# Kernel optimization log

Measured on AMD Instinct MI355X. Metric: run time of the kernel, lower is better.

## Reference

```python
import jax, jax.numpy as jnp
import numpy as np

HEADS = 8
DIM_HEAD = 64
EPS = 1e-05


def _layernorm(t, scale):
    # flax LayerNorm with use_bias=False: (t - mean) / sqrt(var + eps) * scale
    mu = jnp.mean(t, axis=-1, keepdims=True)
    var = jnp.var(t, axis=-1, keepdims=True)
    return (t - mu) * jax.lax.rsqrt(var + EPS) * scale


def setup_inputs() -> dict:
    key = jax.random.key(0)
    ks = jax.random.split(key, 5)
    B, H, W, C = 32, 32, 32, 512
    dim = HEADS * DIM_HEAD  # 512
    x = jax.random.normal(ks[0], (B, H, W, C), dtype=jnp.float32)
    ln1_scale = jnp.ones((C,), dtype=jnp.float32)
    # 1x1 convs == channel matmuls; kernels stored as [in, out]
    w_qkv = jax.random.normal(ks[1], (C, dim * 3), dtype=jnp.float32) * 0.02
    w_out = jax.random.normal(ks[2], (dim, C), dtype=jnp.float32) * 0.02
    b_out = jnp.zeros((C,), dtype=jnp.float32)
    ln2_scale = jnp.ones((C,), dtype=jnp.float32)
    return {"x": x, "ln1_scale": ln1_scale, "w_qkv": w_qkv,
            "w_out": w_out, "b_out": b_out, "ln2_scale": ln2_scale}


def reference(x, ln1_scale, w_qkv, w_out, b_out, ln2_scale):
    B, H, W, C = x.shape
    N = H * W
    dim = HEADS * DIM_HEAD

    normed = _layernorm(x, ln1_scale)                       # [B,H,W,C]
    qkv = jnp.einsum('bxyc,cf->bxyf', normed, w_qkv)        # 1x1 conv, no bias
    q, k, v = jnp.split(qkv, 3, axis=-1)
    q = q.reshape(B, N, HEADS, DIM_HEAD)
    k = k.reshape(B, N, HEADS, DIM_HEAD)
    v = v.reshape(B, N, HEADS, DIM_HEAD)

    q = jax.nn.softmax(q, axis=-1) / jnp.sqrt(jnp.asarray(DIM_HEAD, x.dtype))
    k = jax.nn.softmax(k, axis=1)   # softmax over the token axis (axis=-3)
    v = v / N

    # linear attention: context = k^T v, then out = q . context
    context = jnp.einsum('bnhd,bnhe->bhde', k, v)           # [B,h,d,e]
    out = jnp.einsum('bhde,bnhd->bnhe', context, q)         # == 'b h e n' transposed
    out = out.reshape(B, H, W, dim)

    out = jnp.einsum('bxyf,fc->bxyc', out, w_out) + b_out   # 1x1 conv with bias
    out = _layernorm(out, ln2_scale)                        # to_out.norm_0
    return out + x
```

## Files before the change

kernel.cpp:

```cpp
#include <hip/hip_runtime.h>
#include <stdint.h>

typedef _Float16 h8 __attribute__((ext_vector_type(8)));
typedef _Float16 h4v __attribute__((ext_vector_type(4)));
typedef float f32x4 __attribute__((ext_vector_type(4)));

__device__ __forceinline__ float clampf(float x, float lo, float hi) {
    return fminf(fmaxf(x, lo), hi);
}
__device__ __forceinline__ void gload16(const _Float16* g, _Float16* l) {
    __builtin_amdgcn_global_load_lds(
        (const __attribute__((address_space(1))) unsigned int*)g,
        (__attribute__((address_space(3))) unsigned int*)l, 16, 0, 0);
}

__global__ __launch_bounds__(256) void transpose_f2h(const float* __restrict__ in,
                                                     _Float16* __restrict__ out,
                                                     int rows, int cols) {
    __shared__ _Float16 tile[32][33];
    int bx = blockIdx.x * 32, by = blockIdx.y * 32;
    int tx = threadIdx.x & 31, ty = threadIdx.x >> 5;
    for (int i = ty; i < 32; i += 8)
        tile[i][tx] = (_Float16)in[(size_t)(by + i) * cols + bx + tx];
    __syncthreads();
    for (int i = ty; i < 32; i += 8)
        out[(size_t)(bx + i) * rows + by + tx] = tile[tx][i];
}

__global__ __launch_bounds__(256) void ln1_kernel(const float* __restrict__ x,
                                                  const float* __restrict__ scale,
                                                  _Float16* __restrict__ out) {
    int row = blockIdx.x * 4 + (threadIdx.x >> 6);
    int lane = threadIdx.x & 63;
    const float4* xp = (const float4*)(x + (size_t)row * 512 + lane * 8);
    float4 a = xp[0], b = xp[1];
    const float4* sp = (const float4*)(scale + lane * 8);
    float4 s0v = sp[0], s1v = sp[1];
    float f[8] = {a.x, a.y, a.z, a.w, b.x, b.y, b.z, b.w};
    float sc[8] = {s0v.x, s0v.y, s0v.z, s0v.w, s1v.x, s1v.y, s1v.z, s1v.w};
    float s = 0.f, ss = 0.f;
#pragma unroll
    for (int j = 0; j < 8; j++) { s += f[j]; ss += f[j] * f[j]; }
#pragma unroll
    for (int off = 1; off < 64; off <<= 1) { s += __shfl_xor(s, off); ss += __shfl_xor(ss, off); }
    float mean = s * (1.f / 512.f);
    float var  = ss * (1.f / 512.f) - mean * mean;
    float rs   = rsqrtf(fmaxf(var, 0.f) + 1e-5f);
    union { uint4 u; _Float16 h[8]; } ov;
#pragma unroll
    for (int j = 0; j < 8; j++) ov.h[j] = (_Float16)((f[j] - mean) * rs * sc[j]);
    *(uint4*)(out + (size_t)row * 512 + lane * 8) = ov.u;
}

__global__ __launch_bounds__(512) void gemm_kvexp(const _Float16* __restrict__ A,
                                                  const _Float16* __restrict__ BT,
                                                  _Float16* __restrict__ ekT,
                                                  _Float16* __restrict__ vT,
                                                  float* __restrict__ Sbuf) {
    __shared__ __attribute__((aligned(16))) _Float16 Ws[128 * 32];
    __shared__ __attribute__((aligned(16))) _Float16 Ns[512 * 32];
    int t = threadIdx.x, w = t >> 6, lane = t & 63;
    int lm = lane & 15, q4 = lane >> 4;
    int n0 = blockIdx.x * 512, c0 = blockIdx.y * 128;
    int wc = (w & 1) * 64, wn = (w >> 1) * 128;
    f32x4 acc[4][8];
#pragma unroll
    for (int i = 0; i < 4; i++)
#pragma unroll
        for (int j = 0; j < 8; j++) acc[i][j] = (f32x4){0.f, 0.f, 0.f, 0.f};

    int sr = t >> 2, sc = (t & 3) * 8;
    const _Float16* Wg = BT + (size_t)(c0 + sr) * 512 + sc;
    const _Float16* Ng = A + (size_t)(n0 + sr) * 512 + sc;
    _Float16* WsW = Ws + w * 512;

    for (int k0 = 0; k0 < 512; k0 += 32) {
        gload16(Wg + k0, WsW);
#pragma unroll
        for (int j = 0; j < 4; j++)
            gload16(Ng + (size_t)j * 128 * 512 + k0, Ns + j * 4096 + w * 512);
        __syncthreads();
        h8 wf[4], nf[8];
#pragma unroll
        for (int i = 0; i < 4; i++) wf[i] = *(const h8*)(Ws + (wc + i * 16 + lm) * 32 + q4 * 8);
#pragma unroll
        for (int i = 0; i < 8; i++) nf[i] = *(const h8*)(Ns + (wn + i * 16 + lm) * 32 + q4 * 8);
#pragma unroll
        for (int ci = 0; ci < 4; ci++)
#pragma unroll
            for (int nj = 0; nj < 8; nj++)
                acc[ci][nj] = __builtin_amdgcn_mfma_f32_16x16x32_f16(nf[nj], wf[ci], acc[ci][nj], 0, 0, 0);
        __syncthreads();
    }
    bool isK = (c0 < 512);
    int bl = n0 >> 10;
    int nl0 = (n0 & 1023) + wn;
    _Float16* obase = isK ? ekT : vT;
#pragma unroll
    for (int ci = 0; ci < 4; ci++) {
        int c_abs = c0 + wc + ci * 16 + lm;
        int h = (c_abs >> 6) & 7, de = c_abs & 63;
        _Float16* rowp = obase + ((size_t)(bl * 8 + h) * 64 + de) * 1024 + nl0;
        float ssum = 0.f;
#pragma unroll
        for (int nj = 0; nj < 8; nj++) {
            f32x4 v = acc[ci][nj];
            h4v o;
#pragma unroll
            for (int r = 0; r < 4; r++) {
                float f = v[r];
                if (isK) f = __expf(clampf(f, -30.f, 30.f));
                _Float16 e = (_Float16)f;
                o[r] = e;
                ssum += (float)e;
            }
            *(h4v*)(rowp + nj * 16 + q4 * 4) = o;
        }
        if (isK) {
            ssum += __shfl_xor(ssum, 16);
            ssum += __shfl_xor(ssum, 32);
            if (q4 == 0) atomicAdd(&Sbuf[(bl * 8 + h) * 64 + de], ssum);
        }
    }
}

__global__ __launch_bounds__(512) void ctx_gemm(const _Float16* __restrict__ ekT,
                                                const _Float16* __restrict__ vT,
                                                float* __restrict__ part) {
    __shared__ __attribute__((aligned(16))) _Float16 As[64 * 32];
    __shared__ __attribute__((aligned(16))) _Float16 Bs[64 * 32];
    int t = threadIdx.x, w = t >> 6, lane = t & 63;
    int lm = lane & 15, q4 = lane >> 4;
    int bhl = blockIdx.x;
    int wd = (w & 3) * 16, we = (w >> 2) * 32;
    int tl = t & 255;
    int sr = tl >> 2, sc = (tl & 3) * 8;
    const _Float16* G = (t >= 256 ? vT : ekT) + (size_t)bhl * 65536 + (size_t)sr * 1024 + sc;
    _Float16* LW = (t >= 256 ? Bs : As) + (w & 3) * 512;
    f32x4 acc[2];
    acc[0] = (f32x4){0.f, 0.f, 0.f, 0.f};
    acc[1] = (f32x4){0.f, 0.f, 0.f, 0.f};

    for (int k0 = 0; k0 < 1024; k0 += 32) {
        gload16(G + k0, LW);
        __syncthreads();
        h8 af = *(const h8*)(As + (wd + lm) * 32 + q4 * 8);
#pragma unroll
        for (int nt = 0; nt < 2; nt++) {
            h8 bf = *(const h8*)(Bs + (we + nt * 16 + lm) * 32 + q4 * 8);
            acc[nt] = __builtin_amdgcn_mfma_f32_16x16x32_f16(bf, af, acc[nt], 0, 0, 0);
        }
        __syncthreads();
    }
    float* dst = part + (size_t)bhl * 4096 + (wd + lm) * 64 + we;
#pragma unroll
    for (int nt = 0; nt < 2; nt++)
        *(f32x4*)(dst + nt * 16 + q4 * 4) = acc[nt];
}

__global__ __launch_bounds__(256) void gemm_qattn(const _Float16* __restrict__ A,
                                                  const _Float16* __restrict__ BT,
                                                  const float* __restrict__ part,
                                                  const float* __restrict__ Sbuf,
                                                  _Float16* __restrict__ attn) {
    __shared__ __attribute__((aligned(16))) char smem[33792 + 17408];
    _Float16* As  = (_Float16*)smem;
    _Float16* Bs  = (_Float16*)(smem + 8192);
    _Float16* qn  = (_Float16*)smem;
    _Float16* csT = (_Float16*)(smem + 33792);
    int t = threadIdx.x, w = t >> 6, lane = t & 63;
    int lm = lane & 15, q4 = lane >> 4;
    int m0 = blockIdx.y * 128, n0 = blockIdx.x * 128;
    int wm = (w & 1) * 64, wn = (w >> 1) * 64;
    f32x4 acc[4][4];
#pragma unroll
    for (int i = 0; i < 4; i++)
#pragma unroll
        for (int j = 0; j < 4; j++) acc[i][j] = (f32x4){0.f, 0.f, 0.f, 0.f};

    int sr = t >> 2, sc = (t & 3) * 8;
    const _Float16* Ag = A + (size_t)(m0 + sr) * 512 + sc;
    const _Float16* Bg = BT + (size_t)(n0 + sr) * 512 + sc;
    _Float16* AsW = As + w * 512;
    _Float16* BsW = Bs + w * 512;

    for (int k0 = 0; k0 < 512; k0 += 32) {
        gload16(Ag + k0, AsW);
        gload16(Ag + (size_t)64 * 512 + k0, AsW + 64 * 32);
        gload16(Bg + k0, BsW);
        gload16(Bg + (size_t)64 * 512 + k0, BsW + 64 * 32);
        __syncthreads();
        h8 af[4], bf[4];
#pragma unroll
        for (int i = 0; i < 4; i++) af[i] = *(const h8*)(As + (wm + i * 16 + lm) * 32 + q4 * 8);
#pragma unroll
        for (int i = 0; i < 4; i++) bf[i] = *(const h8*)(Bs + (wn + i * 16 + lm) * 32 + q4 * 8);
#pragma unroll
        for (int mi = 0; mi < 4; mi++)
#pragma unroll
            for (int ni = 0; ni < 4; ni++)
                acc[mi][ni] = __builtin_amdgcn_mfma_f32_16x16x32_f16(bf[ni], af[mi], acc[mi][ni], 0, 0, 0);
        __syncthreads();
    }
    float rws[4];
#pragma unroll
    for (int mi = 0; mi < 4; mi++) {
        float s = 0.f;
#pragma unroll
        for (int ni = 0; ni < 4; ni++) {
            f32x4 e;
#pragma unroll
            for (int r = 0; r < 4; r++) {
                e[r] = __expf(clampf(acc[mi][ni][r], -30.f, 30.f));
                s += e[r];
            }
            acc[mi][ni] = e;
        }
        s += __shfl_xor(s, 16);
        s += __shfl_xor(s, 32);
        rws[mi] = 1.f / (s * 8.f);
    }
#pragma unroll
    for (int mi = 0; mi < 4; mi++) {
        int row = wm + mi * 16 + lm;
        float r = rws[mi];
#pragma unroll
        for (int ni = 0; ni < 4; ni++) {
            int col0 = wn + ni * 16 + q4 * 4;
            h4v o;
#pragma unroll
            for (int j = 0; j < 4; j++) o[j] = (_Float16)(acc[mi][ni][j] * r);
            *(h4v*)(qn + row * 132 + col0) = o;
        }
    }
    int bl = m0 >> 10;
    int head0 = n0 >> 6;
#pragma unroll
    for (int hh2 = 0; hh2 < 2; hh2++) {
        int bh = bl * 8 + head0 + hh2;
        const f32x4* p0 = (const f32x4*)(part + (size_t)bh * 4096);
        for (int i = t; i < 1024; i += 256) {
            f32x4 v = p0[i];
            int d = i >> 4, e0 = (i & 15) * 4;
            float is = 1.f / Sbuf[bh * 64 + d];
#pragma unroll
            for (int j = 0; j < 4; j++)
                csT[hh2 * 64 * 68 + (e0 + j) * 68 + d] = (_Float16)(v[j] * is);
        }
    }
    __syncthreads();
    int hh = w >> 1;
    f32x4 acc2[4][4];
#pragma unroll
    for (int i = 0; i < 4; i++)
#pragma unroll
        for (int j = 0; j < 4; j++) acc2[i][j] = (f32x4){0.f, 0.f, 0.f, 0.f};
#pragma unroll
    for (int kc = 0; kc < 2; kc++) {
        h8 af[4], bf[4];
#pragma unroll
        for (int mi = 0; mi < 4; mi++) {
            const _Float16* p = qn + (wm + mi * 16 + lm) * 132 + hh * 64 + kc * 32 + q4 * 8;
            h4v lo = *(const h4v*)p;
            h4v hi = *(const h4v*)(p + 4);
            h8 a;
#pragma unroll
            for (int j = 0; j < 4; j++) { a[j] = lo[j]; a[4 + j] = hi[j]; }
            af[mi] = a;
        }
#pragma unroll
        for (int ni = 0; ni < 4; ni++) {
            const _Float16* p = csT + hh * 64 * 68 + (ni * 16 + lm) * 68 + kc * 32 + q4 * 8;
            h4v lo = *(const h4v*)p;
            h4v hi = *(const h4v*)(p + 4);
            h8 b;
#pragma unroll
            for (int j = 0; j < 4; j++) { b[j] = lo[j]; b[4 + j] = hi[j]; }
            bf[ni] = b;
        }
#pragma unroll
        for (int mi = 0; mi < 4; mi++)
#pragma unroll
            for (int ni = 0; ni < 4; ni++)
                acc2[mi][ni] = __builtin_amdgcn_mfma_f32_16x16x32_f16(bf[ni], af[mi], acc2[mi][ni], 0, 0, 0);
    }
#pragma unroll
    for (int mi = 0; mi < 4; mi++) {
        int row = m0 + wm + mi * 16 + lm;
#pragma unroll
        for (int ni = 0; ni < 4; ni++) {
            int col0 = n0 + wn + ni * 16 + q4 * 4;
            h4v o;
#pragma unroll
            for (int r = 0; r < 4; r++) o[r] = (_Float16)acc2[mi][ni][r];
            *(h4v*)(attn + (size_t)row * 512 + col0) = o;
        }
    }
}

__global__ __launch_bounds__(512) void gemm_projln2(const _Float16* __restrict__ A,
                                                    const _Float16* __restrict__ BT,
                                                    const float* __restrict__ bias,
                                                    const float* __restrict__ x,
                                                    const float* __restrict__ scale,
                                                    float* __restrict__ out) {
    __shared__ __attribute__((aligned(16))) _Float16 As[128 * 32];
    __shared__ __attribute__((aligned(16))) _Float16 Bs[512 * 32];
    __shared__ float rs_sum[2][64][4];
    __shared__ float rs_ssq[2][64][4];
    int t = threadIdx.x, w = t >> 6, lane = t & 63;
    int lm = lane & 15, q4 = lane >> 4;
    int m0 = blockIdx.x * 128;
    int wm = (w & 1) * 64, wn = (w >> 1) * 128;
    f32x4 acc[4][8];
#pragma unroll
    for (int i = 0; i < 4; i++)
#pragma unroll
        for (int j = 0; j < 8; j++) acc[i][j] = (f32x4){0.f, 0.f, 0.f, 0.f};

    int sr = t >> 2, sc = (t & 3) * 8;
    const _Float16* Ag = A + (size_t)(m0 + sr) * 512 + sc;
    const _Float16* Bg = BT + (size_t)sr * 512 + sc;
    _Float16* AsW = As + w * 512;

    for (int k0 = 0; k0 < 512; k0 += 32) {
        gload16(Ag + k0, AsW);
#pragma unroll
        for (int j = 0; j < 4; j++)
            gload16(Bg + (size_t)j * 128 * 512 + k0, Bs + j * 4096 + w * 512);
        __syncthreads();
        h8 af[4], bf[8];
#pragma unroll
        for (int i = 0; i < 4; i++) af[i] = *(const h8*)(As + (wm + i * 16 + lm) * 32 + q4 * 8);
#pragma unroll
        for (int i = 0; i < 8; i++) bf[i] = *(const h8*)(Bs + (wn + i * 16 + lm) * 32 + q4 * 8);
#pragma unroll
        for (int mi = 0; mi < 4; mi++)
#pragma unroll
            for (int ni = 0; ni < 8; ni++)
                acc[mi][ni] = __builtin_amdgcn_mfma_f32_16x16x32_f16(bf[ni], af[mi], acc[mi][ni], 0, 0, 0);
        __syncthreads();
    }
    const float os = 1.f / 1024.f;
    int mwi = w & 1, nwi = w >> 1;
#pragma unroll
    for (int mi = 0; mi < 4; mi++) {
        float s = 0.f, ss = 0.f;
#pragma unroll
        for (int ni = 0; ni < 8; ni++) {
            float4 b4 = *(const float4*)(bias + wn + ni * 16 + q4 * 4);
            const float* bp = &b4.x;
#pragma unroll
            for (int r = 0; r < 4; r++) {
                float v = acc[mi][ni][r] * os + bp[r];
                acc[mi][ni][r] = v;
                s += v; ss += v * v;
            }
        }
        s  += __shfl_xor(s, 16);  s  += __shfl_xor(s, 32);
        ss += __shfl_xor(ss, 16); ss += __shfl_xor(ss, 32);
        if (q4 == 0) {
            rs_sum[mwi][mi * 16 + lm][nwi] = s;
            rs_ssq[mwi][mi * 16 + lm][nwi] = ss;
        }
    }
    __syncthreads();
#pragma unroll
    for (int mi = 0; mi < 4; mi++) {
        int r64 = mi * 16 + lm;
        float s  = rs_sum[mwi][r64][0] + rs_sum[mwi][r64][1] + rs_sum[mwi][r64][2] + rs_sum[mwi][r64][3];
        float ss = rs_ssq[mwi][r64][0] + rs_ssq[mwi][r64][1] + rs_ssq[mwi][r64][2] + rs_ssq[mwi][r64][3];
        float mean = s * (1.f / 512.f);
        float var  = ss * (1.f / 512.f) - mean * mean;
        float rstd = rsqrtf(fmaxf(var, 0.f) + 1e-5f);
        int row = m0 + wm + r64;
#pragma unroll
        for (int ni = 0; ni < 8; ni++) {
            int col0 = wn + ni * 16 + q4 * 4;
            float4 sc4 = *(const float4*)(scale + col0);
            float4 x4  = *(const float4*)(x + (size_t)row * 512 + col0);
            const float* scp = &sc4.x; const float* xp = &x4.x;
            float4 o;
            float* op = &o.x;
#pragma unroll
            for (int r = 0; r < 4; r++)
                op[r] = (acc[mi][ni][r] - mean) * rstd * scp[r] + xp[r];
            *(float4*)(out + (size_t)row * 512 + col0) = o;
        }
    }
}

extern "C" void kernel_launch(void* const* d_in, const int* in_sizes, int n_in,
                              void* d_out, int out_size, void* d_ws, size_t ws_size,
                              hipStream_t stream) {
    const float* x    = (const float*)d_in[0];
    const float* ln1s = (const float*)d_in[1];
    const float* wqkv = (const float*)d_in[2];
    const float* wout = (const float*)d_in[3];
    const float* bout = (const float*)d_in[4];
    const float* ln2s = (const float*)d_in[5];
    float* out = (float*)d_out;

    char* ws = (char*)d_ws;
    _Float16* wqkvT  = (_Float16*)(ws);
    _Float16* woutT  = (_Float16*)(ws + 1572864);
    float*    part   = (float*)(ws + 2097152);
    float*    Sbuf   = (float*)(ws + 6291456);
    _Float16* normed = (_Float16*)(ws + 6356992);
    _Float16* attnF  = (_Float16*)(ws + 39911424);
    _Float16* ekT = (_Float16*)d_out;
    _Float16* vT  = (_Float16*)((char*)d_out + 33554432);

    transpose_f2h<<<dim3(48, 16), 256, 0, stream>>>(wqkv, wqkvT, 512, 1536);
    transpose_f2h<<<dim3(16, 16), 256, 0, stream>>>(wout, woutT, 512, 512);
    ln1_kernel<<<8192, 256, 0, stream>>>(x, ln1s, normed);
    hipMemsetAsync(Sbuf, 0, 65536, stream);

    gemm_kvexp<<<dim3(64, 8), 512, 0, stream>>>(normed, wqkvT + 512 * 512, ekT, vT, Sbuf);
    ctx_gemm<<<256, 512, 0, stream>>>(ekT, vT, part);
    gemm_qattn<<<dim3(4, 256), 256, 0, stream>>>(normed, wqkvT, part, Sbuf, attnF);
    gemm_projln2<<<256, 512, 0, stream>>>(attnF, woutT, bout, x, ln2s, out);
}
```

Before: 290.7 us.

## Fuse K/V projection with context GemM and shrink projection-LN2 tiles

The K/V projection GEMM now computes exp(k) and v for one batch-head over a 512-token chunk. It writes them as fp16 into shared memory and immediately accumulates the k^T v context with MFMA, so the separate ctx_gemm kernel and the 64 MB fp16 ekT/vT round trip through global memory go away. Each of the two token chunks writes its own context partial, and gemm_qattn sums the two. The output projection + LayerNorm kernel now uses 64-row tiles across 512 blocks instead of 128-row tiles, trading more redundant weight loads for better occupancy and a smaller accumulator footprint. The fused kernel also adds extra barriers and a serialized 4-chunk staging loop in shared memory.

```diff
diff --git a/kernel.cpp b/kernel.cpp
--- a/kernel.cpp
+++ b/kernel.cpp
@@ -52,16 +52,19 @@
     *(uint4*)(out + (size_t)row * 512 + lane * 8) = ov.u;
 }
 
-__global__ __launch_bounds__(512) void gemm_kvexp(const _Float16* __restrict__ A,
+__global__ __launch_bounds__(512) void gemm_kvctx(const _Float16* __restrict__ A,
                                                   const _Float16* __restrict__ BT,
-                                                  _Float16* __restrict__ ekT,
-                                                  _Float16* __restrict__ vT,
+                                                  float* __restrict__ part2,
                                                   float* __restrict__ Sbuf) {
-    __shared__ __attribute__((aligned(16))) _Float16 Ws[128 * 32];
-    __shared__ __attribute__((aligned(16))) _Float16 Ns[512 * 32];
+    __shared__ __attribute__((aligned(16))) char smem[40960];
+    _Float16* Ws = (_Float16*)smem;
+    _Float16* Ns = (_Float16*)(smem + 8192);
+    _Float16* T  = (_Float16*)smem;
     int t = threadIdx.x, w = t >> 6, lane = t & 63;
     int lm = lane & 15, q4 = lane >> 4;
-    int n0 = blockIdx.x * 512, c0 = blockIdx.y * 128;
+    int ns = blockIdx.x, bh = blockIdx.y;
+    int bl = bh >> 3, h = bh & 7;
+    int nr0 = bl * 1024 + ns * 512;
     int wc = (w & 1) * 64, wn = (w >> 1) * 128;
     f32x4 acc[4][8];
 #pragma unroll
@@ -70,8 +73,9 @@
         for (int j = 0; j < 8; j++) acc[i][j] = (f32x4){0.f, 0.f, 0.f, 0.f};
 
     int sr = t >> 2, sc = (t & 3) * 8;
-    const _Float16* Wg = BT + (size_t)(c0 + sr) * 512 + sc;
-    const _Float16* Ng = A + (size_t)(n0 + sr) * 512 + sc;
+    int grow = (sr < 64) ? (h * 64 + sr) : (512 + h * 64 + (sr - 64));
+    const _Float16* Wg = BT + (size_t)grow * 512 + sc;
+    const _Float16* Ng = A + (size_t)(nr0 + sr) * 512 + sc;
     _Float16* WsW = Ws + w * 512;
 
     for (int k0 = 0; k0 < 512; k0 += 32) {
@@ -92,70 +96,71 @@
                 acc[ci][nj] = __builtin_amdgcn_mfma_f32_16x16x32_f16(nf[nj], wf[ci], acc[ci][nj], 0, 0, 0);
         __syncthreads();
     }
-    bool isK = (c0 < 512);
-    int bl = n0 >> 10;
-    int nl0 = (n0 & 1023) + wn;
-    _Float16* obase = isK ? ekT : vT;
-#pragma unroll
-    for (int ci = 0; ci < 4; ci++) {
-        int c_abs = c0 + wc + ci * 16 + lm;
-        int h = (c_abs >> 6) & 7, de = c_abs & 63;
-        _Float16* rowp = obase + ((size_t)(bl * 8 + h) * 64 + de) * 1024 + nl0;
-        float ssum = 0.f;
-#pragma unroll
-        for (int nj = 0; nj < 8; nj++) {
-            f32x4 v = acc[ci][nj];
-            h4v o;
-#pragma unroll
-            for (int r = 0; r < 4; r++) {
-                float f = v[r];
-                if (isK) f = __expf(clampf(f, -30.f, 30.f));
-                _Float16 e = (_Float16)f;
-                o[r] = e;
-                ssum += (float)e;
+    if ((w & 1) == 0) {
+#pragma unroll
+        for (int ci = 0; ci < 4; ci++)
+#pragma unroll
+            for (int nj = 0; nj < 8; nj++) {
+                f32x4 v = acc[ci][nj];
+#pragma unroll
+                for (int r = 0; r < 4; r++) v[r] = __expf(clampf(v[r], -30.f, 30.f));
+                acc[ci][nj] = v;
             }
-            *(h4v*)(rowp + nj * 16 + q4 * 4) = o;
-        }
-        if (isK) {
-            ssum += __shfl_xor(ssum, 16);
-            ssum += __shfl_xor(ssum, 32);
-            if (q4 == 0) atomicAdd(&Sbuf[(bl * 8 + h) * 64 + de], ssum);
-        }
-    }
-}
-
-__global__ __launch_bounds__(512) void ctx_gemm(const _Float16* __restrict__ ekT,
-                                                const _Float16* __restrict__ vT,
-                                                float* __restrict__ part) {
-    __shared__ __attribute__((aligned(16))) _Float16 As[64 * 32];
-    __shared__ __attribute__((aligned(16))) _Float16 Bs[64 * 32];
-    int t = threadIdx.x, w = t >> 6, lane = t & 63;
-    int lm = lane & 15, q4 = lane >> 4;
-    int bhl = blockIdx.x;
+    }
+    int myChunk = w >> 1;
     int wd = (w & 3) * 16, we = (w >> 2) * 32;
-    int tl = t & 255;
-    int sr = tl >> 2, sc = (tl & 3) * 8;
-    const _Float16* G = (t >= 256 ? vT : ekT) + (size_t)bhl * 65536 + (size_t)sr * 1024 + sc;
-    _Float16* LW = (t >= 256 ? Bs : As) + (w & 3) * 512;
-    f32x4 acc[2];
-    acc[0] = (f32x4){0.f, 0.f, 0.f, 0.f};
-    acc[1] = (f32x4){0.f, 0.f, 0.f, 0.f};
-
-    for (int k0 = 0; k0 < 1024; k0 += 32) {
-        gload16(G + k0, LW);
-        __syncthreads();
-        h8 af = *(const h8*)(As + (wd + lm) * 32 + q4 * 8);
-#pragma unroll
-        for (int nt = 0; nt < 2; nt++) {
-            h8 bf = *(const h8*)(Bs + (we + nt * 16 + lm) * 32 + q4 * 8);
-            acc[nt] = __builtin_amdgcn_mfma_f32_16x16x32_f16(bf, af, acc[nt], 0, 0, 0);
-        }
-        __syncthreads();
-    }
-    float* dst = part + (size_t)bhl * 4096 + (wd + lm) * 64 + we;
+    f32x4 acc2[2];
+    acc2[0] = (f32x4){0.f, 0.f, 0.f, 0.f};
+    acc2[1] = (f32x4){0.f, 0.f, 0.f, 0.f};
+    float ssum[4] = {0.f, 0.f, 0.f, 0.f};
+
+#pragma unroll
+    for (int j = 0; j < 4; j++) {
+        if (myChunk == j) {
+            int rbase = (w & 1) * 64;
+#pragma unroll
+            for (int ci = 0; ci < 4; ci++) {
+                float ss = 0.f;
+#pragma unroll
+                for (int nj = 0; nj < 8; nj++) {
+                    f32x4 v = acc[ci][nj];
+                    h4v o;
+#pragma unroll
+                    for (int r = 0; r < 4; r++) {
+                        _Float16 e = (_Float16)v[r];
+                        o[r] = e;
+                        ss += (float)e;
+                    }
+                    *(h4v*)(T + (rbase + ci * 16 + lm) * 136 + nj * 16 + q4 * 4) = o;
+                }
+                ssum[ci] = ss;
+            }
+        }
+        __syncthreads();
+#pragma unroll
+        for (int ks = 0; ks < 4; ks++) {
+            h8 af = *(const h8*)(T + (wd + lm) * 136 + ks * 32 + q4 * 8);
+#pragma unroll
+            for (int nt = 0; nt < 2; nt++) {
+                h8 bf = *(const h8*)(T + (64 + we + nt * 16 + lm) * 136 + ks * 32 + q4 * 8);
+                acc2[nt] = __builtin_amdgcn_mfma_f32_16x16x32_f16(bf, af, acc2[nt], 0, 0, 0);
+            }
+        }
+        __syncthreads();
+    }
+    if ((w & 1) == 0) {
+#pragma unroll
+        for (int ci = 0; ci < 4; ci++) {
+            float s2 = ssum[ci];
+            s2 += __shfl_xor(s2, 16);
+            s2 += __shfl_xor(s2, 32);
+            if (q4 == 0) atomicAdd(&Sbuf[bh * 64 + ci * 16 + lm], s2);
+        }
+    }
+    float* dst = part2 + ((size_t)ns * 256 + bh) * 4096 + (wd + lm) * 64 + we;
 #pragma unroll
     for (int nt = 0; nt < 2; nt++)
-        *(f32x4*)(dst + nt * 16 + q4 * 4) = acc[nt];
+        *(f32x4*)(dst + nt * 16 + q4 * 4) = acc2[nt];
 }
 
 __global__ __launch_bounds__(256) void gemm_qattn(const _Float16* __restrict__ A,
@@ -239,8 +244,9 @@
     for (int hh2 = 0; hh2 < 2; hh2++) {
         int bh = bl * 8 + head0 + hh2;
         const f32x4* p0 = (const f32x4*)(part + (size_t)bh * 4096);
+        const f32x4* p1 = (const f32x4*)(part + (size_t)(256 + bh) * 4096);
         for (int i = t; i < 1024; i += 256) {
-            f32x4 v = p0[i];
+            f32x4 v = p0[i] + p1[i];
             int d = i >> 4, e0 = (i & 15) * 4;
             float is = 1.f / Sbuf[bh * 64 + d];
 #pragma unroll
@@ -304,51 +310,49 @@
                                                     const float* __restrict__ x,
                                                     const float* __restrict__ scale,
                                                     float* __restrict__ out) {
-    __shared__ __attribute__((aligned(16))) _Float16 As[128 * 32];
+    __shared__ __attribute__((aligned(16))) _Float16 As[64 * 32];
     __shared__ __attribute__((aligned(16))) _Float16 Bs[512 * 32];
-    __shared__ float rs_sum[2][64][4];
-    __shared__ float rs_ssq[2][64][4];
+    __shared__ float rs_sum[64][8];
+    __shared__ float rs_ssq[64][8];
     int t = threadIdx.x, w = t >> 6, lane = t & 63;
     int lm = lane & 15, q4 = lane >> 4;
-    int m0 = blockIdx.x * 128;
-    int wm = (w & 1) * 64, wn = (w >> 1) * 128;
-    f32x4 acc[4][8];
+    int m0 = blockIdx.x * 64;
+    f32x4 acc[4][4];
 #pragma unroll
     for (int i = 0; i < 4; i++)
 #pragma unroll
-        for (int j = 0; j < 8; j++) acc[i][j] = (f32x4){0.f, 0.f, 0.f, 0.f};
+        for (int j = 0; j < 4; j++) acc[i][j] = (f32x4){0.f, 0.f, 0.f, 0.f};
 
     int sr = t >> 2, sc = (t & 3) * 8;
-    const _Float16* Ag = A + (size_t)(m0 + sr) * 512 + sc;
+    const _Float16* Ag = A + (size_t)(m0 + (w & 3) * 16 + (lane >> 2)) * 512 + (lane & 3) * 8;
     const _Float16* Bg = BT + (size_t)sr * 512 + sc;
-    _Float16* AsW = As + w * 512;
+    _Float16* AsW = As + (w & 3) * 512;
 
     for (int k0 = 0; k0 < 512; k0 += 32) {
-        gload16(Ag + k0, AsW);
+        if (w < 4) gload16(Ag + k0, AsW);
 #pragma unroll
         for (int j = 0; j < 4; j++)
             gload16(Bg + (size_t)j * 128 * 512 + k0, Bs + j * 4096 + w * 512);
         __syncthreads();
-        h8 af[4], bf[8];
-#pragma unroll
-        for (int i = 0; i < 4; i++) af[i] = *(const h8*)(As + (wm + i * 16 + lm) * 32 + q4 * 8);
-#pragma unroll
-        for (int i = 0; i < 8; i++) bf[i] = *(const h8*)(Bs + (wn + i * 16 + lm) * 32 + q4 * 8);
+        h8 af[4], bf[4];
+#pragma unroll
+        for (int i = 0; i < 4; i++) af[i] = *(const h8*)(As + (i * 16 + lm) * 32 + q4 * 8);
+#pragma unroll
+        for (int i = 0; i < 4; i++) bf[i] = *(const h8*)(Bs + (w * 64 + i * 16 + lm) * 32 + q4 * 8);
 #pragma unroll
         for (int mi = 0; mi < 4; mi++)
 #pragma unroll
-            for (int ni = 0; ni < 8; ni++)
+            for (int ni = 0; ni < 4; ni++)
                 acc[mi][ni] = __builtin_amdgcn_mfma_f32_16x16x32_f16(bf[ni], af[mi], acc[mi][ni], 0, 0, 0);
         __syncthreads();
     }
     const float os = 1.f / 1024.f;
-    int mwi = w & 1, nwi = w >> 1;
 #pragma unroll
     for (int mi = 0; mi < 4; mi++) {
         float s = 0.f, ss = 0.f;
 #pragma unroll
-        for (int ni = 0; ni < 8; ni++) {
-            float4 b4 = *(const float4*)(bias + wn + ni * 16 + q4 * 4);
+        for (int ni = 0; ni < 4; ni++) {
+            float4 b4 = *(const float4*)(bias + w * 64 + ni * 16 + q4 * 4);
             const float* bp = &b4.x;
 #pragma unroll
             for (int r = 0; r < 4; r++) {
@@ -360,23 +364,24 @@
         s  += __shfl_xor(s, 16);  s  += __shfl_xor(s, 32);
         ss += __shfl_xor(ss, 16); ss += __shfl_xor(ss, 32);
         if (q4 == 0) {
-            rs_sum[mwi][mi * 16 + lm][nwi] = s;
-            rs_ssq[mwi][mi * 16 + lm][nwi] = ss;
+            rs_sum[mi * 16 + lm][w] = s;
+            rs_ssq[mi * 16 + lm][w] = ss;
         }
     }
     __syncthreads();
 #pragma unroll
     for (int mi = 0; mi < 4; mi++) {
         int r64 = mi * 16 + lm;
-        float s  = rs_sum[mwi][r64][0] + rs_sum[mwi][r64][1] + rs_sum[mwi][r64][2] + rs_sum[mwi][r64][3];
-        float ss = rs_ssq[mwi][r64][0] + rs_ssq[mwi][r64][1] + rs_ssq[mwi][r64][2] + rs_ssq[mwi][r64][3];
+        float s = 0.f, ss = 0.f;
+#pragma unroll
+        for (int k = 0; k < 8; k++) { s += rs_sum[r64][k]; ss += rs_ssq[r64][k]; }
         float mean = s * (1.f / 512.f);
         float var  = ss * (1.f / 512.f) - mean * mean;
         float rstd = rsqrtf(fmaxf(var, 0.f) + 1e-5f);
-        int row = m0 + wm + r64;
-#pragma unroll
-        for (int ni = 0; ni < 8; ni++) {
-            int col0 = wn + ni * 16 + q4 * 4;
+        int row = m0 + r64;
+#pragma unroll
+        for (int ni = 0; ni < 4; ni++) {
+            int col0 = w * 64 + ni * 16 + q4 * 4;
             float4 sc4 = *(const float4*)(scale + col0);
             float4 x4  = *(const float4*)(x + (size_t)row * 512 + col0);
             const float* scp = &sc4.x; const float* xp = &x4.x;
@@ -404,20 +409,17 @@
     char* ws = (char*)d_ws;
     _Float16* wqkvT  = (_Float16*)(ws);
     _Float16* woutT  = (_Float16*)(ws + 1572864);
-    float*    part   = (float*)(ws + 2097152);
     float*    Sbuf   = (float*)(ws + 6291456);
     _Float16* normed = (_Float16*)(ws + 6356992);
     _Float16* attnF  = (_Float16*)(ws + 39911424);
-    _Float16* ekT = (_Float16*)d_out;
-    _Float16* vT  = (_Float16*)((char*)d_out + 33554432);
+    float* part2 = (float*)d_out;
 
     transpose_f2h<<<dim3(48, 16), 256, 0, stream>>>(wqkv, wqkvT, 512, 1536);
     transpose_f2h<<<dim3(16, 16), 256, 0, stream>>>(wout, woutT, 512, 512);
     ln1_kernel<<<8192, 256, 0, stream>>>(x, ln1s, normed);
     hipMemsetAsync(Sbuf, 0, 65536, stream);
 
-    gemm_kvexp<<<dim3(64, 8), 512, 0, stream>>>(normed, wqkvT + 512 * 512, ekT, vT, Sbuf);
-    ctx_gemm<<<256, 512, 0, stream>>>(ekT, vT, part);
-    gemm_qattn<<<dim3(4, 256), 256, 0, stream>>>(normed, wqkvT, part, Sbuf, attnF);
-    gemm_projln2<<<256, 512, 0, stream>>>(attnF, woutT, bout, x, ln2s, out);
-}
+    gemm_kvctx<<<dim3(2, 256), 512, 0, stream>>>(normed, wqkvT + 512 * 512, part2, Sbuf);
+    gemm_qattn<<<dim3(4, 256), 256, 0, stream>>>(normed, wqkvT, part2, Sbuf, attnF);
+    gemm_projln2<<<512, 512, 0, stream>>>(attnF, woutT, bout, x, ln2s, out);
+}
```

After: 274.9 us. -5.4%, faster.
